# Kernel optimization log

Hardware: AMD Instinct MI355X
Metric: run time of the kernel (lower is better)

Reference implementation:

```python
import jax, jax.numpy as jnp
import numpy as np

B, H, S, D = 2, 12, 4096, 64

def setup_inputs() -> dict:
    key = jax.random.key(0)
    kq, kk, kv = jax.random.split(key, 3)
    Q = jax.random.normal(kq, (B, H, S, D), dtype=jnp.float32)
    K = jax.random.normal(kk, (B, H, S, D), dtype=jnp.float32)
    V = jax.random.normal(kv, (B, H, S, D), dtype=jnp.float32)
    attn_mask = jnp.zeros((1, 1, 1, 1), dtype=bool)  # unused by the original forward
    return {"Q": Q, "K": K, "V": V, "attn_mask": attn_mask}

def reference(Q, K, V, attn_mask):
    d_k = K.shape[3]
    # scores: [B, H, S, S] -- naive full materialization, matching the original
    scores = jnp.einsum("bhqd,bhkd->bhqk", Q, K) / np.sqrt(d_k).astype(Q.dtype)
    attn = jax.nn.softmax(scores, axis=-1)
    context = jnp.einsum("bhqk,bhkd->bhqd", attn, V)
    return context
```

## Files before the change

### kernel.cpp

```cpp
#include <hip/hip_runtime.h>

typedef _Float16 half4_t __attribute__((ext_vector_type(4)));
typedef _Float16 half8_t __attribute__((ext_vector_type(8)));
typedef float floatx4 __attribute__((ext_vector_type(4)));

constexpr int S_  = 4096;
constexpr int D_  = 64;
constexpr int NBH = 24;
constexpr int BM  = 128;
constexpr int BN  = 64;
constexpr int SK  = 72;
constexpr int SV  = 68;
constexpr float SC2 = 0.125f * 1.44269504088896340736f;


__global__ __launch_bounds__(256, 3) void fattn_kernel(
    const float* __restrict__ Q, const float* __restrict__ K,
    const float* __restrict__ V, float* __restrict__ O)
{
  __shared__ __align__(16) _Float16 Ks[2][64 * SK];
  __shared__ __align__(16) _Float16 Vs[2][64 * SV];

  const int tid  = threadIdx.x;
  const int lane = tid & 63;
  const int w    = tid >> 6;
  const int g    = lane >> 4;
  const int m    = lane & 15;

  const int bid  = blockIdx.x;
  const int xcd  = bid & 7;
  const int slot = bid >> 3;
  const int bh   = xcd * 3 + (slot >> 5);
  const int qblk = slot & 31;
  const size_t base = (size_t)bh * S_ * D_;
  const int q0 = qblk * BM + w * 32;

  half8_t qf[2][2];
#pragma unroll
  for (int qt = 0; qt < 2; ++qt)
#pragma unroll
    for (int ks = 0; ks < 2; ++ks) {
      const float4* qp = (const float4*)(Q + base + (size_t)(q0 + qt*16 + m) * D_ + 8*g + 32*ks);
      float4 a = qp[0], b = qp[1];
      half8_t v = { (_Float16)(a.x*SC2),(_Float16)(a.y*SC2),(_Float16)(a.z*SC2),(_Float16)(a.w*SC2),
                    (_Float16)(b.x*SC2),(_Float16)(b.y*SC2),(_Float16)(b.z*SC2),(_Float16)(b.w*SC2) };
      qf[qt][ks] = v;
    }

  floatx4 oacc[2][4];
#pragma unroll
  for (int qt = 0; qt < 2; ++qt)
#pragma unroll
    for (int db = 0; db < 4; ++db) oacc[qt][db] = (floatx4){0.f,0.f,0.f,0.f};
  float lsum[2] = {0.f, 0.f};

  const float* Kb = K + base;
  const float* Vb = V + base;

  float4 kreg[4];
  float  vreg[16];
  const int sL = ((lane >> 2) ^ (lane >> 4)) & 3;

  auto issue = [&](int kt) {
    const float* Kt = Kb + (size_t)kt * BN * D_;
#pragma unroll
    for (int it = 0; it < 2; ++it) {
      int sl  = tid + 256 * it;
      int key = sl >> 3;
      int c8  = (sl & 7) << 3;
      const float4* p = (const float4*)(Kt + (size_t)key * D_ + c8);
      kreg[2*it]   = p[0];
      kreg[2*it+1] = p[1];
    }
    const float* Vt = Vb + (size_t)kt * BN * D_;
#pragma unroll
    for (int it = 0; it < 4; ++it) {
      int kb = it * 16 + (w << 2);
      const float* vp = Vt + (size_t)kb * D_ + lane;
      vreg[4*it+0] = vp[0];
      vreg[4*it+1] = vp[D_];
      vreg[4*it+2] = vp[2*D_];
      vreg[4*it+3] = vp[3*D_];
    }
  };

  auto commit = [&](int buf) {
    _Float16* Kd = Ks[buf];
    _Float16* Vd = Vs[buf];
#pragma unroll
    for (int it = 0; it < 2; ++it) {
      int sl  = tid + 256 * it;
      int key = sl >> 3;
      int c8  = (sl & 7) << 3;
      float4 a = kreg[2*it], b = kreg[2*it+1];
      half8_t h = { (_Float16)a.x,(_Float16)a.y,(_Float16)a.z,(_Float16)a.w,
                    (_Float16)b.x,(_Float16)b.y,(_Float16)b.z,(_Float16)b.w };
      *(half8_t*)(&Kd[key * SK + c8]) = h;
    }
#pragma unroll
    for (int it = 0; it < 4; ++it) {
      half4_t h = { (_Float16)vreg[4*it+0], (_Float16)vreg[4*it+1],
                    (_Float16)vreg[4*it+2], (_Float16)vreg[4*it+3] };
      *(half4_t*)(&Vd[lane * SV + 4 * ((4*it + w) ^ sL)]) = h;
    }
  };

  issue(0);
  commit(0);
  __syncthreads();

  const int s0 = m >> 2;

  for (int kt = 0; kt < S_ / BN; ++kt) {
    const int cur = kt & 1;
    if (kt < 63) issue(kt + 1);

    const _Float16* Kd = Ks[cur];
    const _Float16* Vd = Vs[cur];

    half8_t kf[4][2];
#pragma unroll
    for (int nb = 0; nb < 4; ++nb) {
      kf[nb][0] = *(const half8_t*)(&Kd[(16*nb + m) * SK + 8*g]);
      kf[nb][1] = *(const half8_t*)(&Kd[(16*nb + m) * SK + 8*g + 32]);
    }
    half4_t vf[4][4];
#pragma unroll
    for (int nb = 0; nb < 4; ++nb)
#pragma unroll
      for (int db = 0; db < 4; ++db)
        vf[nb][db] = *(const half4_t*)(&Vd[(16*db + m) * SV + 4 * ((4*nb + g) ^ s0 ^ db)]);

#pragma unroll
    for (int qt = 0; qt < 2; ++qt) {
      floatx4 sacc[4];
#pragma unroll
      for (int nb = 0; nb < 4; ++nb) {
        floatx4 acc = (floatx4){0.f,0.f,0.f,0.f};
        acc = __builtin_amdgcn_mfma_f32_16x16x32_f16(kf[nb][0], qf[qt][0], acc, 0, 0, 0);
        acc = __builtin_amdgcn_mfma_f32_16x16x32_f16(kf[nb][1], qf[qt][1], acc, 0, 0, 0);
        sacc[nb] = acc;
      }
      half4_t pf[4];
      float ls = 0.f;
#pragma unroll
      for (int nb = 0; nb < 4; ++nb) {
        float p0 = __builtin_amdgcn_exp2f(sacc[nb][0]);
        float p1 = __builtin_amdgcn_exp2f(sacc[nb][1]);
        float p2 = __builtin_amdgcn_exp2f(sacc[nb][2]);
        float p3 = __builtin_amdgcn_exp2f(sacc[nb][3]);
        ls += p0 + p1 + p2 + p3;
        half4_t pv = { (_Float16)p0, (_Float16)p1, (_Float16)p2, (_Float16)p3 };
        pf[nb] = pv;
      }
      lsum[qt] += ls;
#pragma unroll
      for (int nb = 0; nb < 4; ++nb)
#pragma unroll
        for (int db = 0; db < 4; ++db)
          oacc[qt][db] = __builtin_amdgcn_mfma_f32_16x16x16f16(pf[nb], vf[nb][db], oacc[qt][db], 0, 0, 0);
    }

    if (kt < 63) commit(1 - cur);
    __syncthreads();
  }

#pragma unroll
  for (int qt = 0; qt < 2; ++qt) {
    float l = lsum[qt];
    l += __shfl_xor(l, 16);
    l += __shfl_xor(l, 32);
    floatx4 linv;
#pragma unroll
    for (int r = 0; r < 4; ++r)
      linv[r] = 1.0f / __shfl(l, (lane & 48) + 4*g + r);
    float* Op = O + base + (size_t)(q0 + qt*16) * D_;
#pragma unroll
    for (int db = 0; db < 4; ++db)
#pragma unroll
      for (int r = 0; r < 4; ++r)
        Op[(size_t)(4*g + r) * D_ + 16*db + m] = oacc[qt][db][r] * linv[r];
  }
}

extern "C" void kernel_launch(void* const* d_in, const int* in_sizes, int n_in,
                              void* d_out, int out_size, void* d_ws, size_t ws_size,
                              hipStream_t stream) {
  const float* Q = (const float*)d_in[0];
  const float* K = (const float*)d_in[1];
  const float* V = (const float*)d_in[2];
  float* Out = (float*)d_out;

  dim3 grid(NBH * (S_ / BM));
  dim3 block(256);
  fattn_kernel<<<grid, block, 0, stream>>>(Q, K, V, Out);
}
```

Baseline: 251.7 us.

## Convert K/V to fp16 at load, deepen register prefetch, and simplify V LDS layout

Global K/V loads are now converted to fp16 right away and held as packed half8 registers in two alternating register stages, so prefetch reaches two tiles ahead and the loop is unrolled by two. The V tile moves to a plain padded layout (stride 72) read with 8-wide LDS loads instead of the XOR-swizzled 4-wide scheme. __syncthreads is replaced by a bare lgkmcnt wait plus s_barrier. The goal is to hide global load latency and cut LDS instruction count, at the cost of more registers and possible LDS bank conflicts without the swizzle.

```diff
diff --git a/kernel.cpp b/kernel.cpp
--- a/kernel.cpp
+++ b/kernel.cpp
@@ -10,8 +10,12 @@
 constexpr int BM  = 128;
 constexpr int BN  = 64;
 constexpr int SK  = 72;
-constexpr int SV  = 68;
+constexpr int SV  = 72;
 constexpr float SC2 = 0.125f * 1.44269504088896340736f;
+
+__device__ __forceinline__ void wg_barrier() {
+  asm volatile("s_waitcnt lgkmcnt(0)\n\ts_barrier" ::: "memory");
+}
 
 
 __global__ __launch_bounds__(256, 3) void fattn_kernel(
@@ -57,67 +61,53 @@
   const float* Kb = K + base;
   const float* Vb = V + base;
 
-  float4 kreg[4];
-  float  vreg[16];
-  const int sL = ((lane >> 2) ^ (lane >> 4)) & 3;
-
-  auto issue = [&](int kt) {
+  const int kkey = tid >> 3;
+  const int kcol = (tid & 7) << 3;
+
+  half8_t kh[2][2];
+  half8_t vh[2][2];
+
+  auto issue = [&](int kt, int s) {
     const float* Kt = Kb + (size_t)kt * BN * D_;
 #pragma unroll
     for (int it = 0; it < 2; ++it) {
-      int sl  = tid + 256 * it;
-      int key = sl >> 3;
-      int c8  = (sl & 7) << 3;
-      const float4* p = (const float4*)(Kt + (size_t)key * D_ + c8);
-      kreg[2*it]   = p[0];
-      kreg[2*it+1] = p[1];
-    }
-    const float* Vt = Vb + (size_t)kt * BN * D_;
-#pragma unroll
-    for (int it = 0; it < 4; ++it) {
-      int kb = it * 16 + (w << 2);
-      const float* vp = Vt + (size_t)kb * D_ + lane;
-      vreg[4*it+0] = vp[0];
-      vreg[4*it+1] = vp[D_];
-      vreg[4*it+2] = vp[2*D_];
-      vreg[4*it+3] = vp[3*D_];
-    }
-  };
-
-  auto commit = [&](int buf) {
-    _Float16* Kd = Ks[buf];
-    _Float16* Vd = Vs[buf];
-#pragma unroll
-    for (int it = 0; it < 2; ++it) {
-      int sl  = tid + 256 * it;
-      int key = sl >> 3;
-      int c8  = (sl & 7) << 3;
-      float4 a = kreg[2*it], b = kreg[2*it+1];
+      const float4* p = (const float4*)(Kt + (size_t)(kkey + 32*it) * D_ + kcol);
+      float4 a = p[0], b = p[1];
       half8_t h = { (_Float16)a.x,(_Float16)a.y,(_Float16)a.z,(_Float16)a.w,
                     (_Float16)b.x,(_Float16)b.y,(_Float16)b.z,(_Float16)b.w };
-      *(half8_t*)(&Kd[key * SK + c8]) = h;
-    }
-#pragma unroll
-    for (int it = 0; it < 4; ++it) {
-      half4_t h = { (_Float16)vreg[4*it+0], (_Float16)vreg[4*it+1],
-                    (_Float16)vreg[4*it+2], (_Float16)vreg[4*it+3] };
-      *(half4_t*)(&Vd[lane * SV + 4 * ((4*it + w) ^ sL)]) = h;
+      kh[s][it] = h;
+    }
+    const float* Vt = Vb + (size_t)kt * BN * D_;
+#pragma unroll
+    for (int j = 0; j < 2; ++j) {
+      half8_t h;
+#pragma unroll
+      for (int q = 0; q < 2; ++q) {
+        int kb = (2*j + q) * 16 + 4*w;
+        const float* vp = Vt + (size_t)kb * D_ + lane;
+        h[4*q+0] = (_Float16)vp[0];
+        h[4*q+1] = (_Float16)vp[D_];
+        h[4*q+2] = (_Float16)vp[2*D_];
+        h[4*q+3] = (_Float16)vp[3*D_];
+      }
+      vh[s][j] = h;
     }
   };
 
-  issue(0);
-  commit(0);
-  __syncthreads();
-
-  const int s0 = m >> 2;
-
-  for (int kt = 0; kt < S_ / BN; ++kt) {
-    const int cur = kt & 1;
-    if (kt < 63) issue(kt + 1);
-
-    const _Float16* Kd = Ks[cur];
-    const _Float16* Vd = Vs[cur];
-
+  auto commit = [&](int buf, int s) {
+    _Float16* Kd = (_Float16*)Ks[buf];
+    _Float16* Vd = (_Float16*)Vs[buf];
+#pragma unroll
+    for (int it = 0; it < 2; ++it)
+      *(half8_t*)(&Kd[(kkey + 32*it) * SK + kcol]) = kh[s][it];
+#pragma unroll
+    for (int j = 0; j < 2; ++j)
+      *(half8_t*)(&Vd[lane * SV + 16*w + 8*j]) = vh[s][j];
+  };
+
+  auto compute = [&](int buf) {
+    const _Float16* Kd = (const _Float16*)Ks[buf];
+    const _Float16* Vd = (const _Float16*)Vs[buf];
     half8_t kf[4][2];
 #pragma unroll
     for (int nb = 0; nb < 4; ++nb) {
@@ -126,10 +116,13 @@
     }
     half4_t vf[4][4];
 #pragma unroll
-    for (int nb = 0; nb < 4; ++nb)
-#pragma unroll
-      for (int db = 0; db < 4; ++db)
-        vf[nb][db] = *(const half4_t*)(&Vd[(16*db + m) * SV + 4 * ((4*nb + g) ^ s0 ^ db)]);
+    for (int db = 0; db < 4; ++db)
+#pragma unroll
+      for (int p = 0; p < 2; ++p) {
+        half8_t v8 = *(const half8_t*)(&Vd[(16*db + m) * SV + 16*g + 8*p]);
+        vf[2*p  ][db] = (half4_t){v8[0], v8[1], v8[2], v8[3]};
+        vf[2*p+1][db] = (half4_t){v8[4], v8[5], v8[6], v8[7]};
+      }
 
 #pragma unroll
     for (int qt = 0; qt < 2; ++qt) {
@@ -150,8 +143,7 @@
         float p2 = __builtin_amdgcn_exp2f(sacc[nb][2]);
         float p3 = __builtin_amdgcn_exp2f(sacc[nb][3]);
         ls += p0 + p1 + p2 + p3;
-        half4_t pv = { (_Float16)p0, (_Float16)p1, (_Float16)p2, (_Float16)p3 };
-        pf[nb] = pv;
+        pf[nb] = (half4_t){ (_Float16)p0, (_Float16)p1, (_Float16)p2, (_Float16)p3 };
       }
       lsum[qt] += ls;
 #pragma unroll
@@ -160,9 +152,22 @@
         for (int db = 0; db < 4; ++db)
           oacc[qt][db] = __builtin_amdgcn_mfma_f32_16x16x16f16(pf[nb], vf[nb][db], oacc[qt][db], 0, 0, 0);
     }
-
-    if (kt < 63) commit(1 - cur);
-    __syncthreads();
+  };
+
+  issue(0, 0);
+  commit(0, 0);
+  issue(1, 1);
+  wg_barrier();
+
+  for (int kt = 0; kt < S_ / BN; kt += 2) {
+    if (kt + 2 < S_ / BN) issue(kt + 2, 0);
+    compute(0);
+    commit(1, 1);
+    wg_barrier();
+    if (kt + 3 < S_ / BN) issue(kt + 3, 1);
+    compute(1);
+    if (kt + 2 < S_ / BN) commit(0, 0);
+    wg_barrier();
   }
 
 #pragma unroll
```

After: 579.5 us. +130.3%, slower.
